# Optimization experiments

Measured on AMD Instinct MI355X. Metric: run time of the kernel, lower is better.

The kernel has to match this reference:

```python
import jax, jax.numpy as jnp
import numpy as np

R, K, CF, HF, WF = 64, 81, 256, 256, 256  # ROIs, classes(incl bg), FPN channels, P2 size
IMG = 1024.0
SCALE = 0.25          # P2 feature stride 4
STEPS = 4             # subdivision steps: 7 -> 112
NPTS = 28 * 28        # subdivision_num_points
FC = 256


def _grid_sample(img, coords):
    """torch.grid_sample(bilinear, align_corners=False, zeros padding).
    img: [N,C,H,W]; coords: [N,P,2] (x,y) in [0,1]. Returns [N,C,P]."""
    N, C, H, W = img.shape
    x = coords[..., 0] * W - 0.5
    y = coords[..., 1] * H - 0.5
    x0 = jnp.floor(x); y0 = jnp.floor(y)
    fx = x - x0; fy = y - y0

    def g(ix, iy, w):
        valid = (ix >= 0) & (ix < W) & (iy >= 0) & (iy < H)
        ixc = jnp.clip(ix, 0, W - 1).astype(jnp.int32)
        iyc = jnp.clip(iy, 0, H - 1).astype(jnp.int32)
        v = jax.vmap(lambda im, yy, xx: im[:, yy, xx])(img, iyc, ixc)  # [N,C,P]
        return v * (w * valid)[:, None, :]

    return (g(x0, y0, (1 - fx) * (1 - fy)) + g(x0 + 1, y0, fx * (1 - fy))
            + g(x0, y0 + 1, (1 - fx) * fy) + g(x0 + 1, y0 + 1, fx * fy))


def _point_head(fine, coarse, W1, b1, W2, b2, W3, b3, Wp, bp):
    # StandardPointHead: 1x1-conv fc layers, coarse logits re-concatenated each layer
    x = jnp.concatenate([fine, coarse], axis=1)  # [R, CF+K, P]
    for Wl, bl in ((W1, b1), (W2, b2), (W3, b3)):
        x = jax.nn.relu(jnp.einsum('oc,rcp->rop', Wl, x) + bl[None, :, None])
        x = jnp.concatenate([x, coarse], axis=1)
    return jnp.einsum('oc,rcp->rop', Wp, x) + bp[None, :, None]  # [R,K,P]


def setup_inputs() -> dict:
    key = jax.random.key(0)
    ks = jax.random.split(key, 12)
    feat = jax.random.normal(ks[0], (1, CF, HF, WF), dtype=jnp.float32)
    u = jax.random.uniform(ks[1], (R, 4), dtype=jnp.float32)
    x0 = u[:, 0] * (IMG - 256.0); y0 = u[:, 1] * (IMG - 256.0)
    w = 32.0 + u[:, 2] * 224.0;   h = 32.0 + u[:, 3] * 224.0
    det_bboxes = jnp.stack([x0, y0, x0 + w, y0 + h], axis=1)
    det_labels = jax.random.randint(ks[2], (R,), 0, 80, dtype=jnp.int32)
    coarse_logits = jax.random.normal(ks[3], (R, K, 7, 7), dtype=jnp.float32)
    cin = CF + K  # = FC + K = 337 for all layers here
    s = 0.02
    return {
        'feat': feat, 'det_bboxes': det_bboxes, 'det_labels': det_labels,
        'coarse_logits': coarse_logits,
        'W1': jax.random.normal(ks[4], (FC, cin), jnp.float32) * s,
        'b1': jnp.zeros((FC,), jnp.float32),
        'W2': jax.random.normal(ks[5], (FC, FC + K), jnp.float32) * s,
        'b2': jnp.zeros((FC,), jnp.float32),
        'W3': jax.random.normal(ks[6], (FC, FC + K), jnp.float32) * s,
        'b3': jnp.zeros((FC,), jnp.float32),
        'Wp': jax.random.normal(ks[7], (K, FC + K), jnp.float32) * s,
        'bp': jnp.zeros((K,), jnp.float32),
    }


def reference(feat, det_bboxes, det_labels, coarse_logits,
              W1, b1, W2, b2, W3, b3, Wp, bp):
    ml = coarse_logits
    bx0, by0 = det_bboxes[:, 0], det_bboxes[:, 1]
    bw = det_bboxes[:, 2] - det_bboxes[:, 0]
    bh = det_bboxes[:, 3] - det_bboxes[:, 1]
    for step in range(STEPS):
        _, _, H, W = ml.shape
        H, W = 2 * H, 2 * W
        # bilinear x2, align_corners=False (half-pixel centers)
        ml = jax.image.resize(ml, (R, K, H, W), method='linear')
        if NPTS >= 4 * H * W and step < STEPS - 1:
            continue
        # uncertainty = -|logit of gt class| (det_labels+1 skips background ch 0)
        gt = ml[jnp.arange(R), det_labels + 1]              # [R,H,W]
        unc = -jnp.abs(gt).reshape(R, H * W)
        _, idx = jax.lax.top_k(unc, NPTS)                   # [R,NPTS]
        px = ((idx % W).astype(ml.dtype) + 0.5) / W
        py = ((idx // W).astype(ml.dtype) + 0.5) / H
        coords = jnp.stack([px, py], axis=-1)               # [R,NPTS,2] in ROI [0,1]
        # project ROI coords to image, then to P2 normalized coords
        cx = bx0[:, None] + coords[..., 0] * bw[:, None]
        cy = by0[:, None] + coords[..., 1] * bh[:, None]
        fcoords = jnp.stack([cx * SCALE / WF, cy * SCALE / HF], axis=-1)
        fine = _grid_sample(feat, fcoords.reshape(1, R * NPTS, 2))  # [1,CF,R*NPTS]
        fine = fine[0].reshape(CF, R, NPTS).transpose(1, 0, 2)      # [R,CF,NPTS]
        coarse = _grid_sample(coarse_logits, coords)                # [R,K,NPTS]
        pl = _point_head(fine, coarse, W1, b1, W2, b2, W3, b3, Wp, bp)
        ml = jax.vmap(lambda m, i, p: m.at[:, i].set(p))(
            ml.reshape(R, K, H * W), idx, pl).reshape(R, K, H, W)
    return ml
```

## Files before the change

kernel.cpp:

```cpp
#include <hip/hip_runtime.h>
#include <hip/hip_bf16.h>
#include <cstdint>
#include <cstddef>

#define R_ 64
#define K_ 81
#define NPTS_ 784

typedef __attribute__((ext_vector_type(8))) short short8;
typedef __attribute__((ext_vector_type(4))) float f32x4;

#define GLDS16(G, L)                                                           \
  __builtin_amdgcn_global_load_lds(                                            \
      (__attribute__((address_space(1))) void*)(void*)(G),                     \
      (__attribute__((address_space(3))) void*)(L), 16, 0, 0)

__global__ __launch_bounds__(256) void transpose_feat_kernel(const float* __restrict__ in,
                                                             float* __restrict__ out) {
  __shared__ float tile[32][33];
  int y = blockIdx.z;
  int x0 = blockIdx.x * 32, c0 = blockIdx.y * 32;
  int tx = threadIdx.x, ty = threadIdx.y;
#pragma unroll
  for (int j = 0; j < 32; j += 8)
    tile[ty + j][tx] = in[(size_t)(c0 + ty + j) * 65536 + (size_t)y * 256 + x0 + tx];
  __syncthreads();
#pragma unroll
  for (int j = 0; j < 32; j += 8)
    out[((size_t)y * 256 + (x0 + ty + j)) * 256 + c0 + tx] = tile[tx][ty + j];
}

__global__ void transpose_coarse_kernel(const float* __restrict__ in, float* __restrict__ out) {
  int t = blockIdx.x * 256 + threadIdx.x;
  if (t >= R_ * 49 * K_) return;
  int k = t % K_;
  int t2 = t / K_;
  int pos = t2 % 49;
  int r = t2 / 49;
  out[t] = in[((size_t)r * K_ + k) * 49 + pos];
}

__global__ void prep_wpack_kernel(const float* __restrict__ W1, const float* __restrict__ W2,
                                  const float* __restrict__ W3, const float* __restrict__ Wp,
                                  const float* __restrict__ b1, const float* __restrict__ b2,
                                  const float* __restrict__ b3, const float* __restrict__ bp,
                                  __hip_bfloat16* __restrict__ Wpk, float* __restrict__ bias_all) {
  int t = blockIdx.x * 256 + threadIdx.x;
  if (t < 90112) {
    int lane = t & 63;
    int t2 = t >> 6;
    int hl = t2 & 1;
    t2 >>= 1;
    int jg = t2 & 15;
    t2 >>= 4;
    int kt = t2 % 11;
    int L = t2 / 11;
    int o = jg * 16 + (lane & 15);
    int kbase = kt * 32 + (lane >> 4) * 8;
    const float* Wsrc = (L == 0) ? W1 : (L == 1) ? W2 : (L == 2) ? W3 : Wp;
    int Omax = (L == 3) ? 81 : 256;
    __hip_bfloat16 outv[8];
#pragma unroll
    for (int e = 0; e < 8; ++e) {
      int k = kbase + e;
      float v = (o < Omax && k < 337) ? Wsrc[o * 337 + k] : 0.f;
      __hip_bfloat16 h = __float2bfloat16(v);
      outv[e] = hl ? __float2bfloat16(v - __bfloat162float(h)) : h;
    }
    *(short8*)(Wpk + (size_t)t * 8) = *(const short8*)outv;
  } else if (t < 90112 + 1024) {
    int k = t - 90112;
    float v = 0.f;
    if (k < 256) v = b1[k];
    else if (k < 512) v = b2[k - 256];
    else if (k < 768) v = b3[k - 512];
    else if (k < 768 + 81) v = bp[k - 768];
    bias_all[k] = v;
  }
}

__global__ __launch_bounds__(128) void upsample2x_kernel(const float* __restrict__ in,
                                                         float* __restrict__ out,
                                                         int Hin, int Win) {
  int b = blockIdx.z;
  int iy = blockIdx.y * 2 + threadIdx.y;
  int ix = blockIdx.x * 64 + threadIdx.x;
  if (ix >= Win || iy >= Hin) return;
  const float* p = in + (size_t)b * Hin * Win;
  int rT = (iy == 0) ? 0 : iy - 1;
  int rB = (iy == Hin - 1) ? iy : iy + 1;
  int cL = (ix == 0) ? 0 : ix - 1;
  int cR = (ix == Win - 1) ? ix : ix + 1;
  float wyT1 = (iy == 0) ? 0.f : 0.75f;
  float wyB1 = (iy == Hin - 1) ? 0.f : 0.25f;
  float wxE1 = (ix == 0) ? 0.f : 0.75f;
  float wxO1 = (ix == Win - 1) ? 0.f : 0.25f;
  float wyT0 = 1.f - wyT1, wyB0 = 1.f - wyB1;
  float wxE0 = 1.f - wxE1, wxO0 = 1.f - wxO1;

  const float* rowA = p + (size_t)rT * Win;
  const float* rowM = p + (size_t)iy * Win;
  const float* rowC = p + (size_t)rB * Win;
  float al = rowA[cL], am = rowA[ix], ar = rowA[cR];
  float mL = rowM[cL], mm = rowM[ix], mr = rowM[cR];
  float cl = rowC[cL], cm = rowC[ix], cr = rowC[cR];

  float aE = wxE0 * al + wxE1 * am;
  float aO = wxO0 * am + wxO1 * ar;
  float mE = wxE0 * mL + wxE1 * mm;
  float mO = wxO0 * mm + wxO1 * mr;
  float cE = wxE0 * cl + wxE1 * cm;
  float cO = wxO0 * cm + wxO1 * cr;

  float oTE = wyT0 * aE + wyT1 * mE;
  float oTO = wyT0 * aO + wyT1 * mO;
  float oBE = wyB0 * mE + wyB1 * cE;
  float oBO = wyB0 * mO + wyB1 * cO;

  int Wout = 2 * Win;
  float* ob = out + ((size_t)b * (2 * Hin) + 2 * iy) * Wout + 2 * ix;
  *(float2*)ob = make_float2(oTE, oTO);
  *(float2*)(ob + Wout) = make_float2(oBE, oBO);
}

__global__ void iota_kernel(int* __restrict__ sel) {
  int t = blockIdx.x * 256 + threadIdx.x;
  if (t < R_ * NPTS_) sel[t] = t % NPTS_;
}

__global__ __launch_bounds__(256) void topk_kernel(const float* __restrict__ ml,
                                                   const int* __restrict__ labels,
                                                   int N, int* __restrict__ sel) {
  int r = blockIdx.x;
  const float* gt = ml + ((size_t)r * K_ + (labels[r] + 1)) * N;
  __shared__ unsigned int hist[256];
  __shared__ unsigned int sh_prefix, sh_remaining, sh_countless;
  int tid = threadIdx.x;

  unsigned int prefix = 0;
  unsigned int remaining = NPTS_;
  unsigned int count_less = 0;
  for (int pass = 0; pass < 4; ++pass) {
    int shift = 24 - 8 * pass;
    hist[tid] = 0;
    __syncthreads();
    for (int i = tid; i < N; i += 256) {
      unsigned int v = __float_as_uint(fabsf(gt[i]));
      bool match = (pass == 0) || ((v >> (shift + 8)) == prefix);
      if (match) atomicAdd(&hist[(v >> shift) & 255u], 1u);
    }
    __syncthreads();
    if (tid == 0) {
      unsigned int cum = 0, before = 0;
      int d = 255;
      for (int dd = 0; dd < 256; ++dd) {
        unsigned int c = hist[dd];
        if (cum + c >= remaining) { before = cum; d = dd; break; }
        cum += c;
      }
      sh_prefix = (prefix << 8) | (unsigned int)d;
      sh_remaining = remaining - before;
      sh_countless = count_less + before;
    }
    __syncthreads();
    prefix = sh_prefix;
    remaining = sh_remaining;
    count_less = sh_countless;
    __syncthreads();
  }
  unsigned int vstar = prefix;
  unsigned int need_eq = NPTS_ - count_less;

  __shared__ unsigned int wtot_less[4], wtot_eq[4];
  unsigned int base_less = 0, base_eq = 0;
  int lane = tid & 63, wv = tid >> 6;
  int* selr = sel + (size_t)r * NPTS_;
  for (int base = 0; base < N; base += 256) {
    int i = base + tid;
    bool less = false, eq = false;
    if (i < N) {
      unsigned int v = __float_as_uint(fabsf(gt[i]));
      less = v < vstar;
      eq = v == vstar;
    }
    unsigned long long ml_ = __ballot(less);
    unsigned long long me_ = __ballot(eq);
    unsigned long long lanemask = (lane == 0) ? 0ull : ((~0ull) >> (64 - lane));
    unsigned int pl = __popcll(ml_ & lanemask);
    unsigned int pe = __popcll(me_ & lanemask);
    if (lane == 0) { wtot_less[wv] = (unsigned int)__popcll(ml_); wtot_eq[wv] = (unsigned int)__popcll(me_); }
    __syncthreads();
    unsigned int off_l = 0, off_e = 0, tot_l = 0, tot_e = 0;
#pragma unroll
    for (int w2 = 0; w2 < 4; ++w2) {
      unsigned int tl = wtot_less[w2], te = wtot_eq[w2];
      if (w2 < wv) { off_l += tl; off_e += te; }
      tot_l += tl;
      tot_e += te;
    }
    if (less) selr[base_less + off_l + pl] = i;
    if (eq) {
      unsigned int er = base_eq + off_e + pe;
      if (er < need_eq) selr[count_less + er] = i;
    }
    base_less += tot_l;
    base_eq += tot_e;
    __syncthreads();
  }
}

__global__ __launch_bounds__(256) void sample_kernel(const int* __restrict__ sel,
                                                     const float* __restrict__ bboxes,
                                                     const float* __restrict__ featT,
                                                     const float* __restrict__ coarseT,
                                                     __hip_bfloat16* __restrict__ Xh,
                                                     __hip_bfloat16* __restrict__ Xl,
                                                     __hip_bfloat16* __restrict__ Cth,
                                                     __hip_bfloat16* __restrict__ Ctl,
                                                     int Wlev, int Hlev) {
  int rp = blockIdx.x;
  int r = rp / NPTS_;
  int idx = sel[rp];
  int tid = threadIdx.x;

  float px = ((float)(idx % Wlev) + 0.5f) / (float)Wlev;
  float py = ((float)(idx / Wlev) + 0.5f) / (float)Hlev;
  float bx0 = bboxes[r * 4 + 0], by0 = bboxes[r * 4 + 1];
  float bw = __fsub_rn(bboxes[r * 4 + 2], bx0);
  float bh = __fsub_rn(bboxes[r * 4 + 3], by0);
  float cx = __fadd_rn(bx0, __fmul_rn(px, bw));
  float cy = __fadd_rn(by0, __fmul_rn(py, bh));

  {
    float gx = __fsub_rn(__fmul_rn(cx, 0.25f), 0.5f);
    float gy = __fsub_rn(__fmul_rn(cy, 0.25f), 0.5f);
    float fxf = floorf(gx), fyf = floorf(gy);
    float fx = __fsub_rn(gx, fxf), fy = __fsub_rn(gy, fyf);
    int x0 = (int)fxf, y0 = (int)fyf;
    float ofx = __fsub_rn(1.f, fx), ofy = __fsub_rn(1.f, fy);
    float w00 = __fmul_rn(ofx, ofy);
    float w10 = __fmul_rn(fx, ofy);
    float w01 = __fmul_rn(ofx, fy);
    float w11 = __fmul_rn(fx, fy);
    bool vx0 = (x0 >= 0) && (x0 < 256), vx1 = (x0 + 1 >= 0) && (x0 + 1 < 256);
    bool vy0 = (y0 >= 0) && (y0 < 256), vy1 = (y0 + 1 >= 0) && (y0 + 1 < 256);
    float W00 = (vx0 && vy0) ? w00 : 0.f;
    float W10 = (vx1 && vy0) ? w10 : 0.f;
    float W01 = (vx0 && vy1) ? w01 : 0.f;
    float W11 = (vx1 && vy1) ? w11 : 0.f;
    int x0c = min(max(x0, 0), 255), x1c = min(max(x0 + 1, 0), 255);
    int y0c = min(max(y0, 0), 255), y1c = min(max(y0 + 1, 0), 255);
    const float* p00 = featT + ((size_t)(y0c * 256 + x0c)) * 256;
    const float* p10 = featT + ((size_t)(y0c * 256 + x1c)) * 256;
    const float* p01 = featT + ((size_t)(y1c * 256 + x0c)) * 256;
    const float* p11 = featT + ((size_t)(y1c * 256 + x1c)) * 256;
    float acc = __fmul_rn(p00[tid], W00);
    acc = __fadd_rn(acc, __fmul_rn(p10[tid], W10));
    acc = __fadd_rn(acc, __fmul_rn(p01[tid], W01));
    acc = __fadd_rn(acc, __fmul_rn(p11[tid], W11));
    __hip_bfloat16 h = __float2bfloat16(acc);
    Xh[(size_t)rp * 256 + tid] = h;
    Xl[(size_t)rp * 256 + tid] = __float2bfloat16(acc - __bfloat162float(h));
  }

  if (tid < 96) {
    float acc = 0.f;
    if (tid < K_) {
      float gx = __fsub_rn(__fmul_rn(px, 7.f), 0.5f);
      float gy = __fsub_rn(__fmul_rn(py, 7.f), 0.5f);
      float fxf = floorf(gx), fyf = floorf(gy);
      float fx = __fsub_rn(gx, fxf), fy = __fsub_rn(gy, fyf);
      int x0 = (int)fxf, y0 = (int)fyf;
      float ofx = __fsub_rn(1.f, fx), ofy = __fsub_rn(1.f, fy);
      float w00 = __fmul_rn(ofx, ofy);
      float w10 = __fmul_rn(fx, ofy);
      float w01 = __fmul_rn(ofx, fy);
      float w11 = __fmul_rn(fx, fy);
      bool vx0 = (x0 >= 0) && (x0 < 7), vx1 = (x0 + 1 >= 0) && (x0 + 1 < 7);
      bool vy0 = (y0 >= 0) && (y0 < 7), vy1 = (y0 + 1 >= 0) && (y0 + 1 < 7);
      float W00 = (vx0 && vy0) ? w00 : 0.f;
      float W10 = (vx1 && vy0) ? w10 : 0.f;
      float W01 = (vx0 && vy1) ? w01 : 0.f;
      float W11 = (vx1 && vy1) ? w11 : 0.f;
      int x0c = min(max(x0, 0), 6), x1c = min(max(x0 + 1, 0), 6);
      int y0c = min(max(y0, 0), 6), y1c = min(max(y0 + 1, 0), 6);
      const float* cb = coarseT + (size_t)r * 49 * K_;
      acc = __fmul_rn(cb[(size_t)(y0c * 7 + x0c) * K_ + tid], W00);
      acc = __fadd_rn(acc, __fmul_rn(cb[(size_t)(y0c * 7 + x1c) * K_ + tid], W10));
      acc = __fadd_rn(acc, __fmul_rn(cb[(size_t)(y1c * 7 + x0c) * K_ + tid], W01));
      acc = __fadd_rn(acc, __fmul_rn(cb[(size_t)(y1c * 7 + x1c) * K_ + tid], W11));
    }
    __hip_bfloat16 h = __float2bfloat16(acc);
    Cth[(size_t)rp * 96 + tid] = h;
    Ctl[(size_t)rp * 96 + tid] = __float2bfloat16(acc - __bfloat162float(h));
  }
}

template <int TERMS>
__global__ __launch_bounds__(256, 2) void fused_head_kernel(
    const __hip_bfloat16* __restrict__ Ah, const __hip_bfloat16* __restrict__ Al,
    const __hip_bfloat16* __restrict__ Th, const __hip_bfloat16* __restrict__ Tl,
    const __hip_bfloat16* __restrict__ Wpk,
    const float* __restrict__ bias_all, float* __restrict__ PL) {
  constexpr int XPLANE = 11 * 4096;
  constexpr int XLO = 8 * 4096;
  __shared__ char lds[(TERMS == 3) ? XPLANE + XLO : XPLANE];
  char* Xh = lds;
  char* Xl = lds + XPLANE;

  const int tid = threadIdx.x;
  const int lane = tid & 63;
  const int w = tid >> 6;
  const int g = lane >> 4;
  const int lane15 = lane & 15;
  const int m0 = blockIdx.x * 64;

  {
    const int srow = tid >> 2;
    const int sp = tid & 3;
    const int sx = sp ^ ((srow >> 1) & 3);
#pragma unroll
    for (int kt = 0; kt < 8; ++kt) {
      size_t off = (((size_t)(m0 + srow)) * 256 + (size_t)kt * 32 + (size_t)sx * 8) * 2;
      GLDS16((const char*)Ah + off, Xh + kt * 4096 + w * 1024);
      if constexpr (TERMS == 3) GLDS16((const char*)Al + off, Xl + kt * 4096 + w * 1024);
    }
#pragma unroll
    for (int kt = 8; kt < 11; ++kt) {
      size_t off = (((size_t)(m0 + srow)) * 96 + (size_t)(kt - 8) * 32 + (size_t)sx * 8) * 2;
      GLDS16((const char*)Th + off, Xh + kt * 4096 + w * 1024);
    }
  }
  asm volatile("s_waitcnt vmcnt(0)" ::: "memory");
  __syncthreads();

  int offA[4];
#pragma unroll
  for (int i = 0; i < 4; ++i) {
    int rowA = i * 16 + lane15;
    offA[i] = rowA * 64 + ((g ^ ((rowA >> 1) & 3)) << 4);
  }

#pragma unroll 1
  for (int L = 0; L < 4; ++L) {
    if (L == 3 && w >= 2) break;
    const __hip_bfloat16* WL = Wpk + (size_t)L * (11 * 16 * 2 * 512);

    f32x4 acc[4][4];
#pragma unroll
    for (int i = 0; i < 4; ++i)
#pragma unroll
      for (int j = 0; j < 4; ++j) acc[i][j] = (f32x4){0.f, 0.f, 0.f, 0.f};

    short8 a_h[2][4], a_l[2][4], b_h[2][4], b_l[2][4];
#pragma unroll
    for (int i = 0; i < 4; ++i) {
      a_h[0][i] = *(const short8*)(Xh + offA[i]);
      if constexpr (TERMS == 3) a_l[0][i] = *(const short8*)(Xl + offA[i]);
    }
#pragma unroll
    for (int j = 0; j < 4; ++j) {
      const __hip_bfloat16* bp = WL + (((size_t)0 * 16 + (w * 4 + j)) * 2) * 512 + (size_t)lane * 8;
      b_h[0][j] = *(const short8*)bp;
      if constexpr (TERMS == 3) b_l[0][j] = *(const short8*)(bp + 512);
    }

#pragma unroll
    for (int kt = 0; kt < 11; ++kt) {
      const int c = kt & 1, n = c ^ 1;
      if (kt < 10) {
        const int ktn = kt + 1;
#pragma unroll
        for (int i = 0; i < 4; ++i) {
          a_h[n][i] = *(const short8*)(Xh + ktn * 4096 + offA[i]);
          if constexpr (TERMS == 3) {
            if (ktn < 8)
              a_l[n][i] = *(const short8*)(Xl + ktn * 4096 + offA[i]);
            else
              a_l[n][i] = *(const short8*)((const char*)Tl +
                  (((size_t)(m0 + i * 16 + lane15)) * 96 + (size_t)(ktn - 8) * 32 +
                   (size_t)g * 8) * 2);
          }
        }
#pragma unroll
        for (int j = 0; j < 4; ++j) {
          const __hip_bfloat16* bp =
              WL + (((size_t)ktn * 16 + (w * 4 + j)) * 2) * 512 + (size_t)lane * 8;
          b_h[n][j] = *(const short8*)bp;
          if constexpr (TERMS == 3) b_l[n][j] = *(const short8*)(bp + 512);
        }
      }
#pragma unroll
      for (int i = 0; i < 4; ++i)
#pragma unroll
        for (int j = 0; j < 4; ++j) {
          acc[i][j] = __builtin_amdgcn_mfma_f32_16x16x32_bf16(a_h[c][i], b_h[c][j], acc[i][j], 0, 0, 0);
          if constexpr (TERMS == 3) {
            acc[i][j] = __builtin_amdgcn_mfma_f32_16x16x32_bf16(a_h[c][i], b_l[c][j], acc[i][j], 0, 0, 0);
            acc[i][j] = __builtin_amdgcn_mfma_f32_16x16x32_bf16(a_l[c][i], b_h[c][j], acc[i][j], 0, 0, 0);
          }
        }
    }

    if (L < 3) {
      __syncthreads();
#pragma unroll
      for (int j = 0; j < 4; ++j) {
        int o = w * 64 + j * 16 + lane15;
        float bv = bias_all[L * 256 + o];
        int kch = o >> 5;
        int s0 = (o >> 3) & 3;
        int e = o & 7;
#pragma unroll
        for (int i = 0; i < 4; ++i) {
          int mb = i * 16 + g * 4;
#pragma unroll
          for (int r = 0; r < 4; ++r) {
            int m = mb + r;
            float v = fmaxf(acc[i][j][r] + bv, 0.f);
            __hip_bfloat16 h = __float2bfloat16(v);
            int boff = kch * 4096 + m * 64 + ((s0 ^ ((m >> 1) & 3)) << 4) + e * 2;
            *(__hip_bfloat16*)(Xh + boff) = h;
            if constexpr (TERMS == 3)
              *(__hip_bfloat16*)(Xl + boff) = __float2bfloat16(v - __bfloat162float(h));
          }
        }
      }
      __syncthreads();
    } else {
#pragma unroll
      for (int j = 0; j < 4; ++j) {
        int o = w * 64 + j * 16 + lane15;
        float bv = bias_all[768 + o];
#pragma unroll
        for (int i = 0; i < 4; ++i) {
          int mb = i * 16 + g * 4;
#pragma unroll
          for (int r = 0; r < 4; ++r)
            PL[(size_t)(m0 + mb + r) * 128 + o] = acc[i][j][r] + bv;
        }
      }
    }
  }
}

__global__ void scatter_kernel(const float* __restrict__ PL, const int* __restrict__ sel,
                               float* __restrict__ ml, int Nlev) {
  int t = blockIdx.x * 256 + threadIdx.x;
  if (t >= R_ * NPTS_ * K_) return;
  int k = t % K_;
  int rp = t / K_;
  int i = sel[rp];
  int r = rp / NPTS_;
  ml[((size_t)r * K_ + k) * Nlev + i] = PL[(size_t)rp * 128 + k];
}

extern "C" void kernel_launch(void* const* d_in, const int* in_sizes, int n_in,
                              void* d_out, int out_size, void* d_ws, size_t ws_size,
                              hipStream_t stream) {
  (void)in_sizes; (void)n_in; (void)out_size; (void)ws_size;
  const float* feat = (const float*)d_in[0];
  const float* bboxes = (const float*)d_in[1];
  const int* labels = (const int*)d_in[2];
  const float* coarse = (const float*)d_in[3];
  const float* W1 = (const float*)d_in[4];
  const float* b1 = (const float*)d_in[5];
  const float* W2 = (const float*)d_in[6];
  const float* b2 = (const float*)d_in[7];
  const float* W3 = (const float*)d_in[8];
  const float* b3 = (const float*)d_in[9];
  const float* Wp = (const float*)d_in[10];
  const float* bp = (const float*)d_in[11];
  float* out = (float*)d_out;

  char* p = (char*)d_ws;
  auto alloc = [&](size_t bytes) { char* r = p; p += (bytes + 255) & ~(size_t)255; return r; };
  float* featT = (float*)alloc(16777216ull * 4);
  float* coarseT = (float*)alloc(254016ull * 4);
  float* ml14 = (float*)alloc(1016064ull * 4);
  float* ml28 = (float*)alloc(4064256ull * 4);
  float* ml56 = (float*)alloc(16257024ull * 4);
  float* PL = (float*)alloc(6422528ull * 4);
  int* sel = (int*)alloc(50176ull * 4);
  __hip_bfloat16* Xa_h = (__hip_bfloat16*)alloc(12845056ull * 2);
  __hip_bfloat16* Xa_l = (__hip_bfloat16*)alloc(12845056ull * 2);
  __hip_bfloat16* Ct_h = (__hip_bfloat16*)alloc(4816896ull * 2);
  __hip_bfloat16* Ct_l = (__hip_bfloat16*)alloc(4816896ull * 2);
  __hip_bfloat16* Wpk = (__hip_bfloat16*)alloc(720896ull * 2);
  float* bias_all = (float*)alloc(1024ull * 4);

  const int N = R_ * NPTS_;
  const int B = R_ * K_;

  transpose_feat_kernel<<<dim3(8, 8, 256), dim3(32, 8), 0, stream>>>(feat, featT);
  transpose_coarse_kernel<<<3969, 256, 0, stream>>>(coarse, coarseT);
  prep_wpack_kernel<<<357, 256, 0, stream>>>(W1, W2, W3, Wp, b1, b2, b3, bp, Wpk, bias_all);

  upsample2x_kernel<<<dim3(1, 4, B), dim3(64, 2), 0, stream>>>(coarse, ml14, 7, 7);

  upsample2x_kernel<<<dim3(1, 7, B), dim3(64, 2), 0, stream>>>(ml14, ml28, 14, 14);
  iota_kernel<<<196, 256, 0, stream>>>(sel);
  sample_kernel<<<N, 256, 0, stream>>>(sel, bboxes, featT, coarseT, Xa_h, Xa_l, Ct_h, Ct_l, 28, 28);
  fused_head_kernel<3><<<784, 256, 0, stream>>>(Xa_h, Xa_l, Ct_h, Ct_l, Wpk, bias_all, PL);
  scatter_kernel<<<15876, 256, 0, stream>>>(PL, sel, ml28, 784);

  upsample2x_kernel<<<dim3(1, 14, B), dim3(64, 2), 0, stream>>>(ml28, ml56, 28, 28);
  topk_kernel<<<R_, 256, 0, stream>>>(ml56, labels, 3136, sel);
  sample_kernel<<<N, 256, 0, stream>>>(sel, bboxes, featT, coarseT, Xa_h, Xa_l, Ct_h, Ct_l, 56, 56);
  fused_head_kernel<3><<<784, 256, 0, stream>>>(Xa_h, Xa_l, Ct_h, Ct_l, Wpk, bias_all, PL);
  scatter_kernel<<<15876, 256, 0, stream>>>(PL, sel, ml56, 3136);

  upsample2x_kernel<<<dim3(1, 28, B), dim3(64, 2), 0, stream>>>(ml56, out, 56, 56);
  topk_kernel<<<R_, 256, 0, stream>>>(out, labels, 12544, sel);
  sample_kernel<<<N, 256, 0, stream>>>(sel, bboxes, featT, coarseT, Xa_h, Xa_l, Ct_h, Ct_l, 112, 112);
  fused_head_kernel<1><<<784, 256, 0, stream>>>(Xa_h, nullptr, Ct_h, nullptr, Wpk, bias_all, PL);
  scatter_kernel<<<15876, 256, 0, stream>>>(PL, sel, out, 12544);
}
```

Before: 919.2 us.

## Split fused head into 8 waves over row halves with single-buffered A loads

The fused point-head kernel now runs 512 threads per block. Eight waves split the 64-row tile into two 32-row halves, and each half is covered by four column groups, which halves the accumulator and A-register footprint per wave. The initial LDS staging is split across the two thread halves. A fragments are now loaded per k-step without double buffering, and the MFMA section is wrapped in s_setprio. The aim is more waves for latency hiding and lower register pressure, at the cost of each wave reloading the B weights redundantly and more barrier participants.

```diff
diff --git a/kernel.cpp b/kernel.cpp
--- a/kernel.cpp
+++ b/kernel.cpp
@@ -297,7 +297,7 @@
 }
 
 template <int TERMS>
-__global__ __launch_bounds__(256, 2) void fused_head_kernel(
+__global__ __launch_bounds__(512, 2) void fused_head_kernel(
     const __hip_bfloat16* __restrict__ Ah, const __hip_bfloat16* __restrict__ Al,
     const __hip_bfloat16* __restrict__ Th, const __hip_bfloat16* __restrict__ Tl,
     const __hip_bfloat16* __restrict__ Wpk,
@@ -311,109 +311,136 @@
   const int tid = threadIdx.x;
   const int lane = tid & 63;
   const int w = tid >> 6;
+  const int pg = w >> 2;
+  const int cg = w & 3;
   const int g = lane >> 4;
   const int lane15 = lane & 15;
   const int m0 = blockIdx.x * 64;
 
   {
-    const int srow = tid >> 2;
-    const int sp = tid & 3;
+    const int half = tid >> 8;
+    const int t2 = tid & 255;
+    const int w4 = t2 >> 6;
+    const int srow = t2 >> 2;
+    const int sp = t2 & 3;
     const int sx = sp ^ ((srow >> 1) & 3);
-#pragma unroll
-    for (int kt = 0; kt < 8; ++kt) {
-      size_t off = (((size_t)(m0 + srow)) * 256 + (size_t)kt * 32 + (size_t)sx * 8) * 2;
-      GLDS16((const char*)Ah + off, Xh + kt * 4096 + w * 1024);
-      if constexpr (TERMS == 3) GLDS16((const char*)Al + off, Xl + kt * 4096 + w * 1024);
-    }
-#pragma unroll
-    for (int kt = 8; kt < 11; ++kt) {
-      size_t off = (((size_t)(m0 + srow)) * 96 + (size_t)(kt - 8) * 32 + (size_t)sx * 8) * 2;
-      GLDS16((const char*)Th + off, Xh + kt * 4096 + w * 1024);
+    if constexpr (TERMS == 3) {
+      if (half == 0) {
+#pragma unroll
+        for (int kt = 0; kt < 8; ++kt) {
+          size_t off = (((size_t)(m0 + srow)) * 256 + (size_t)kt * 32 + (size_t)sx * 8) * 2;
+          GLDS16((const char*)Ah + off, Xh + kt * 4096 + w4 * 1024);
+        }
+#pragma unroll
+        for (int kt = 8; kt < 11; ++kt) {
+          size_t off = (((size_t)(m0 + srow)) * 96 + (size_t)(kt - 8) * 32 + (size_t)sx * 8) * 2;
+          GLDS16((const char*)Th + off, Xh + kt * 4096 + w4 * 1024);
+        }
+      } else {
+#pragma unroll
+        for (int kt = 0; kt < 8; ++kt) {
+          size_t off = (((size_t)(m0 + srow)) * 256 + (size_t)kt * 32 + (size_t)sx * 8) * 2;
+          GLDS16((const char*)Al + off, Xl + kt * 4096 + w4 * 1024);
+        }
+      }
+    } else {
+      if (half == 0) {
+#pragma unroll
+        for (int kt = 0; kt < 6; ++kt) {
+          size_t off = (((size_t)(m0 + srow)) * 256 + (size_t)kt * 32 + (size_t)sx * 8) * 2;
+          GLDS16((const char*)Ah + off, Xh + kt * 4096 + w4 * 1024);
+        }
+      } else {
+#pragma unroll
+        for (int kt = 6; kt < 8; ++kt) {
+          size_t off = (((size_t)(m0 + srow)) * 256 + (size_t)kt * 32 + (size_t)sx * 8) * 2;
+          GLDS16((const char*)Ah + off, Xh + kt * 4096 + w4 * 1024);
+        }
+#pragma unroll
+        for (int kt = 8; kt < 11; ++kt) {
+          size_t off = (((size_t)(m0 + srow)) * 96 + (size_t)(kt - 8) * 32 + (size_t)sx * 8) * 2;
+          GLDS16((const char*)Th + off, Xh + kt * 4096 + w4 * 1024);
+        }
+      }
     }
   }
   asm volatile("s_waitcnt vmcnt(0)" ::: "memory");
   __syncthreads();
 
-  int offA[4];
-#pragma unroll
-  for (int i = 0; i < 4; ++i) {
-    int rowA = i * 16 + lane15;
+  int offA[2];
+#pragma unroll
+  for (int i = 0; i < 2; ++i) {
+    int rowA = pg * 32 + i * 16 + lane15;
     offA[i] = rowA * 64 + ((g ^ ((rowA >> 1) & 3)) << 4);
   }
 
 #pragma unroll 1
   for (int L = 0; L < 4; ++L) {
-    if (L == 3 && w >= 2) break;
+    if (L == 3 && cg >= 2) break;
     const __hip_bfloat16* WL = Wpk + (size_t)L * (11 * 16 * 2 * 512);
 
-    f32x4 acc[4][4];
-#pragma unroll
-    for (int i = 0; i < 4; ++i)
+    f32x4 acc[2][4];
+#pragma unroll
+    for (int i = 0; i < 2; ++i)
 #pragma unroll
       for (int j = 0; j < 4; ++j) acc[i][j] = (f32x4){0.f, 0.f, 0.f, 0.f};
 
-    short8 a_h[2][4], a_l[2][4], b_h[2][4], b_l[2][4];
-#pragma unroll
-    for (int i = 0; i < 4; ++i) {
-      a_h[0][i] = *(const short8*)(Xh + offA[i]);
-      if constexpr (TERMS == 3) a_l[0][i] = *(const short8*)(Xl + offA[i]);
-    }
-#pragma unroll
-    for (int j = 0; j < 4; ++j) {
-      const __hip_bfloat16* bp = WL + (((size_t)0 * 16 + (w * 4 + j)) * 2) * 512 + (size_t)lane * 8;
-      b_h[0][j] = *(const short8*)bp;
-      if constexpr (TERMS == 3) b_l[0][j] = *(const short8*)(bp + 512);
-    }
+    short8 a_h[2], a_l[2], b_h[2][4], b_l[2][4];
+
+    auto loadB = [&](int buf, int kt) {
+#pragma unroll
+      for (int j = 0; j < 4; ++j) {
+        const __hip_bfloat16* bp =
+            WL + (((size_t)kt * 16 + (cg * 4 + j)) * 2) * 512 + (size_t)lane * 8;
+        b_h[buf][j] = *(const short8*)bp;
+        if constexpr (TERMS == 3) b_l[buf][j] = *(const short8*)(bp + 512);
+      }
+    };
+
+    loadB(0, 0);
 
 #pragma unroll
     for (int kt = 0; kt < 11; ++kt) {
-      const int c = kt & 1, n = c ^ 1;
-      if (kt < 10) {
-        const int ktn = kt + 1;
-#pragma unroll
-        for (int i = 0; i < 4; ++i) {
-          a_h[n][i] = *(const short8*)(Xh + ktn * 4096 + offA[i]);
+      const int cb = kt & 1;
+      if (kt < 10) loadB(cb ^ 1, kt + 1);
+#pragma unroll
+      for (int i = 0; i < 2; ++i) {
+        a_h[i] = *(const short8*)(Xh + kt * 4096 + offA[i]);
+        if constexpr (TERMS == 3) {
+          if (kt < 8)
+            a_l[i] = *(const short8*)(Xl + kt * 4096 + offA[i]);
+          else
+            a_l[i] = *(const short8*)((const char*)Tl +
+                (((size_t)(m0 + pg * 32 + i * 16 + lane15)) * 96 +
+                 (size_t)(kt - 8) * 32 + (size_t)g * 8) * 2);
+        }
+      }
+      __builtin_amdgcn_s_setprio(1);
+#pragma unroll
+      for (int i = 0; i < 2; ++i)
+#pragma unroll
+        for (int j = 0; j < 4; ++j) {
+          acc[i][j] = __builtin_amdgcn_mfma_f32_16x16x32_bf16(a_h[i], b_h[cb][j], acc[i][j], 0, 0, 0);
           if constexpr (TERMS == 3) {
-            if (ktn < 8)
-              a_l[n][i] = *(const short8*)(Xl + ktn * 4096 + offA[i]);
-            else
-              a_l[n][i] = *(const short8*)((const char*)Tl +
-                  (((size_t)(m0 + i * 16 + lane15)) * 96 + (size_t)(ktn - 8) * 32 +
-                   (size_t)g * 8) * 2);
+            acc[i][j] = __builtin_amdgcn_mfma_f32_16x16x32_bf16(a_h[i], b_l[cb][j], acc[i][j], 0, 0, 0);
+            acc[i][j] = __builtin_amdgcn_mfma_f32_16x16x32_bf16(a_l[i], b_h[cb][j], acc[i][j], 0, 0, 0);
           }
         }
-#pragma unroll
-        for (int j = 0; j < 4; ++j) {
-          const __hip_bfloat16* bp =
-              WL + (((size_t)ktn * 16 + (w * 4 + j)) * 2) * 512 + (size_t)lane * 8;
-          b_h[n][j] = *(const short8*)bp;
-          if constexpr (TERMS == 3) b_l[n][j] = *(const short8*)(bp + 512);
-        }
-      }
-#pragma unroll
-      for (int i = 0; i < 4; ++i)
-#pragma unroll
-        for (int j = 0; j < 4; ++j) {
-          acc[i][j] = __builtin_amdgcn_mfma_f32_16x16x32_bf16(a_h[c][i], b_h[c][j], acc[i][j], 0, 0, 0);
-          if constexpr (TERMS == 3) {
-            acc[i][j] = __builtin_amdgcn_mfma_f32_16x16x32_bf16(a_h[c][i], b_l[c][j], acc[i][j], 0, 0, 0);
-            acc[i][j] = __builtin_amdgcn_mfma_f32_16x16x32_bf16(a_l[c][i], b_h[c][j], acc[i][j], 0, 0, 0);
-          }
-        }
+      __builtin_amdgcn_s_setprio(0);
     }
 
     if (L < 3) {
       __syncthreads();
 #pragma unroll
       for (int j = 0; j < 4; ++j) {
-        int o = w * 64 + j * 16 + lane15;
+        int o = cg * 64 + j * 16 + lane15;
         float bv = bias_all[L * 256 + o];
         int kch = o >> 5;
         int s0 = (o >> 3) & 3;
         int e = o & 7;
 #pragma unroll
-        for (int i = 0; i < 4; ++i) {
-          int mb = i * 16 + g * 4;
+        for (int i = 0; i < 2; ++i) {
+          int mb = pg * 32 + i * 16 + g * 4;
 #pragma unroll
           for (int r = 0; r < 4; ++r) {
             int m = mb + r;
@@ -430,14 +457,14 @@
     } else {
 #pragma unroll
       for (int j = 0; j < 4; ++j) {
-        int o = w * 64 + j * 16 + lane15;
+        int o = cg * 64 + j * 16 + lane15;
         float bv = bias_all[768 + o];
 #pragma unroll
-        for (int i = 0; i < 4; ++i) {
-          int mb = i * 16 + g * 4;
+        for (int i = 0; i < 2; ++i) {
+          int mb = m0 + pg * 32 + i * 16 + g * 4;
 #pragma unroll
           for (int r = 0; r < 4; ++r)
-            PL[(size_t)(m0 + mb + r) * 128 + o] = acc[i][j][r] + bv;
+            PL[(size_t)(mb + r) * 128 + o] = acc[i][j][r] + bv;
         }
       }
     }
@@ -501,18 +528,18 @@
   upsample2x_kernel<<<dim3(1, 7, B), dim3(64, 2), 0, stream>>>(ml14, ml28, 14, 14);
   iota_kernel<<<196, 256, 0, stream>>>(sel);
   sample_kernel<<<N, 256, 0, stream>>>(sel, bboxes, featT, coarseT, Xa_h, Xa_l, Ct_h, Ct_l, 28, 28);
-  fused_head_kernel<3><<<784, 256, 0, stream>>>(Xa_h, Xa_l, Ct_h, Ct_l, Wpk, bias_all, PL);
+  fused_head_kernel<3><<<784, 512, 0, stream>>>(Xa_h, Xa_l, Ct_h, Ct_l, Wpk, bias_all, PL);
   scatter_kernel<<<15876, 256, 0, stream>>>(PL, sel, ml28, 784);
 
   upsample2x_kernel<<<dim3(1, 14, B), dim3(64, 2), 0, stream>>>(ml28, ml56, 28, 28);
   topk_kernel<<<R_, 256, 0, stream>>>(ml56, labels, 3136, sel);
   sample_kernel<<<N, 256, 0, stream>>>(sel, bboxes, featT, coarseT, Xa_h, Xa_l, Ct_h, Ct_l, 56, 56);
-  fused_head_kernel<3><<<784, 256, 0, stream>>>(Xa_h, Xa_l, Ct_h, Ct_l, Wpk, bias_all, PL);
+  fused_head_kernel<3><<<784, 512, 0, stream>>>(Xa_h, Xa_l, Ct_h, Ct_l, Wpk, bias_all, PL);
   scatter_kernel<<<15876, 256, 0, stream>>>(PL, sel, ml56, 3136);
 
   upsample2x_kernel<<<dim3(1, 28, B), dim3(64, 2), 0, stream>>>(ml56, out, 56, 56);
   topk_kernel<<<R_, 256, 0, stream>>>(out, labels, 12544, sel);
   sample_kernel<<<N, 256, 0, stream>>>(sel, bboxes, featT, coarseT, Xa_h, Xa_l, Ct_h, Ct_l, 112, 112);
-  fused_head_kernel<1><<<784, 256, 0, stream>>>(Xa_h, nullptr, Ct_h, nullptr, Wpk, bias_all, PL);
+  fused_head_kernel<1><<<784, 512, 0, stream>>>(Xa_h, nullptr, Ct_h, nullptr, Wpk, bias_all, PL);
   scatter_kernel<<<15876, 256, 0, stream>>>(PL, sel, out, 12544);
 }
```

Result: no change. 913.7 us (-0.6%).
